# Kernel optimization log

Measured on AMD Instinct MI355X. Metric: run time of the kernel, lower is better.

## Reference

```python
import jax, jax.numpy as jnp
import numpy as np

EMBED = 1024
HEADS = 16
HIDDEN = 4 * EMBED
EPS = 1e-5


def layer_norm(x, g, b):
    mu = jnp.mean(x, axis=-1, keepdims=True)
    var = jnp.var(x, axis=-1, keepdims=True)
    return (x - mu) * jax.lax.rsqrt(var + EPS) * g + b


def setup_inputs() -> dict:
    key = jax.random.key(0)
    ks = jax.random.split(key, 8)
    s = EMBED ** -0.5
    return {
        "x": jax.random.normal(ks[0], (4, 2048, EMBED), dtype=jnp.float32),
        "ln1_g": jnp.ones((EMBED,), jnp.float32),
        "ln1_b": jnp.zeros((EMBED,), jnp.float32),
        "qkv_w": jax.random.normal(ks[1], (3 * EMBED, EMBED), jnp.float32) * s,
        "out_w": jax.random.normal(ks[2], (EMBED, EMBED), jnp.float32) * s,
        "out_b": jnp.zeros((EMBED,), jnp.float32),
        "ln2_g": jnp.ones((EMBED,), jnp.float32),
        "ln2_b": jnp.zeros((EMBED,), jnp.float32),
        "fc1_w": jax.random.normal(ks[3], (HIDDEN, EMBED), jnp.float32) * s,
        "fc1_b": jnp.zeros((HIDDEN,), jnp.float32),
        "fc2_w": jax.random.normal(ks[4], (EMBED, HIDDEN), jnp.float32) * (HIDDEN ** -0.5),
        "fc2_b": jnp.zeros((EMBED,), jnp.float32),
    }


def reference(x, ln1_g, ln1_b, qkv_w, out_w, out_b, ln2_g, ln2_b, fc1_w, fc1_b, fc2_w, fc2_b):
    B, N, C = x.shape
    hd = C // HEADS
    # --- attention (pre-LN); note: NO 1/sqrt(d) scaling, matching the source ---
    h = layer_norm(x, ln1_g, ln1_b)
    qkv = h @ qkv_w.T                                  # [B,N,3C]
    qkv = qkv.reshape(B, N, 3, HEADS, hd).transpose(2, 0, 3, 1, 4)
    q, k, v = qkv[0], qkv[1], qkv[2]                   # [B,H,N,hd]
    attn = jax.nn.softmax(jnp.einsum("bhqd,bhkd->bhqk", q, k), axis=-1)
    o = jnp.einsum("bhqk,bhkd->bhqd", attn, v)
    o = o.transpose(0, 2, 1, 3).reshape(B, N, C)
    x = x + o @ out_w.T + out_b
    # --- MLP (exact erf GELU, matching nn.GELU default) ---
    h = layer_norm(x, ln2_g, ln2_b)
    h = jax.nn.gelu(h @ fc1_w.T + fc1_b, approximate=False)
    x = x + h @ fc2_w.T + fc2_b
    return x
```

## Files before the change

kernel.cpp:

```cpp
#include <hip/hip_runtime.h>
#include <cstdint>


using short8 = __attribute__((ext_vector_type(8))) short;
using f32x4  = __attribute__((ext_vector_type(4))) float;
using f32x16 = __attribute__((ext_vector_type(16))) float;

#define EMBED  1024
#define HIDDEN 4096
#define SEQ    2048
#define NTOK   8192

__device__ __forceinline__ ushort f2bf(float x) {
  union { float f; uint32_t u; } v; v.f = x;
  uint32_t r = v.u + 0x7fffu + ((v.u >> 16) & 1u);
  return (ushort)(r >> 16);
}

__device__ __forceinline__ uint32_t pkbf(float lo, float hi) {
  uint32_t r;
  asm("v_cvt_pk_bf16_f32 %0, %1, %2" : "=v"(r) : "v"(lo), "v"(hi));
  return r;
}

__device__ __forceinline__ void gload16(const void* g, void* l) {
  __builtin_amdgcn_global_load_lds((__attribute__((address_space(1))) void*)(g),
                                   (__attribute__((address_space(3))) void*)(l), 16, 0, 0);
}

template<int N> __device__ __forceinline__ void vwait() {
  asm volatile("s_waitcnt vmcnt(%0)" :: "n"(N) : "memory");
}
__device__ __forceinline__ void fence_bar() {
  asm volatile("" ::: "memory");
  __builtin_amdgcn_s_barrier();
  asm volatile("" ::: "memory");
}

__device__ __forceinline__ f32x4 mfma16(short8 a, short8 b, f32x4 c) {
  return __builtin_amdgcn_mfma_f32_16x16x32_bf16(a, b, c, 0, 0, 0);
}
__device__ __forceinline__ f32x16 mfma32(short8 a, short8 b, f32x16 c) {
  return __builtin_amdgcn_mfma_f32_32x32x16_bf16(a, b, c, 0, 0, 0);
}
__device__ __forceinline__ f32x16 zero16() {
  f32x16 z = {0.f,0.f,0.f,0.f,0.f,0.f,0.f,0.f,0.f,0.f,0.f,0.f,0.f,0.f,0.f,0.f};
  return z;
}

__global__ __launch_bounds__(256) void cvt_bf16_kernel(const float* __restrict__ in,
                                                       ushort* __restrict__ out, int n4) {
  int i = blockIdx.x * 256 + threadIdx.x;
  if (i < n4) {
    float4 v = reinterpret_cast<const float4*>(in)[i];
    ushort4 o; o.x = f2bf(v.x); o.y = f2bf(v.y); o.z = f2bf(v.z); o.w = f2bf(v.w);
    reinterpret_cast<ushort4*>(out)[i] = o;
  }
}

__global__ __launch_bounds__(256) void ln_kernel(const float* __restrict__ x,
                                                 const float* __restrict__ g,
                                                 const float* __restrict__ b,
                                                 ushort* __restrict__ out) {
  const int row = blockIdx.x, tid = threadIdx.x;
  const float4 xv = reinterpret_cast<const float4*>(x + (size_t)row * EMBED)[tid];
  float s  = xv.x + xv.y + xv.z + xv.w;
  float s2 = xv.x*xv.x + xv.y*xv.y + xv.z*xv.z + xv.w*xv.w;
  #pragma unroll
  for (int off = 32; off >= 1; off >>= 1) { s += __shfl_xor(s, off); s2 += __shfl_xor(s2, off); }
  __shared__ float ps[4], ps2[4];
  if ((tid & 63) == 0) { ps[tid >> 6] = s; ps2[tid >> 6] = s2; }
  __syncthreads();
  s  = ps[0] + ps[1] + ps[2] + ps[3];
  s2 = ps2[0] + ps2[1] + ps2[2] + ps2[3];
  const float mu  = s * (1.f / EMBED);
  const float var = s2 * (1.f / EMBED) - mu * mu;
  const float rs  = rsqrtf(var + 1e-5f);
  const float4 gv = reinterpret_cast<const float4*>(g)[tid];
  const float4 bv = reinterpret_cast<const float4*>(b)[tid];
  ushort4 o;
  o.x = f2bf((xv.x - mu) * rs * gv.x + bv.x);
  o.y = f2bf((xv.y - mu) * rs * gv.y + bv.y);
  o.z = f2bf((xv.z - mu) * rs * gv.z + bv.z);
  o.w = f2bf((xv.w - mu) * rs * gv.w + bv.w);
  reinterpret_cast<ushort4*>(out + (size_t)row * EMBED)[tid] = o;
}

template<int EPI, bool SQ>
__global__ __launch_bounds__(512) void gemm256(const ushort* __restrict__ A,
                                               const ushort* __restrict__ B,
                                               const float* __restrict__ bias,
                                               const float* __restrict__ res,
                                               ushort* __restrict__ outb,
                                               float* __restrict__ outf,
                                               int M, int N, int K, int gx) {
  constexpr int BN   = SQ ? 256 : 128;
  constexpr int MP   = SQ ? 8 : 4;
  constexpr int NPH  = SQ ? 2 : 1;
  constexpr int LPT  = SQ ? 4 : 3;
  constexpr int NB   = LPT - 2;
  constexpr int ABUF = 256 * 32;
  constexpr int BBUF = BN * 32;
  __shared__ ushort lds[4][ABUF + BBUF];

  const int nwg = gridDim.x;
  const int b0  = blockIdx.x;
  const int bid = (b0 & 7) * (nwg >> 3) + (b0 >> 3);
  const int m0  = (bid % gx) * 256;
  const int n0  = (bid / gx) * BN;

  const int tid = threadIdx.x, lane = tid & 63, wave = tid >> 6;
  const int wm = (SQ ? (wave >> 2) : (wave >> 1)) * (MP * 16);
  const int wn = (SQ ? (wave & 3) : (wave & 1)) * 64;
  const int l15 = lane & 15, l4 = lane >> 4;
  const int NT = K >> 5;

  const ushort* aSrc[2];
  const ushort* bSrc[NB];
  #pragma unroll
  for (int rd = 0; rd < 2; ++rd) {
    const int slot = rd * 512 + tid;
    const int r = slot >> 2;
    const int cs = (slot & 3) ^ ((r >> 1) & 3);
    aSrc[rd] = A + (size_t)(m0 + r) * K + cs * 8;
  }
  #pragma unroll
  for (int rd = 0; rd < NB; ++rd) {
    const int slot = rd * 512 + tid;
    const int r = slot >> 2;
    const int cs = (slot & 3) ^ ((r >> 1) & 3);
    bSrc[rd] = B + (size_t)(n0 + r) * K + cs * 8;
  }
  auto stageA = [&](int buf, int rd) { gload16(aSrc[rd], &lds[buf][(rd * 512 + tid) * 8]); };
  auto stageB = [&](int buf, int rd) { gload16(bSrc[rd], &lds[buf][ABUF + (rd * 512 + tid) * 8]); };
  auto advance = [&]() {
    #pragma unroll
    for (int rd = 0; rd < 2; ++rd) aSrc[rd] += 32;
    #pragma unroll
    for (int rd = 0; rd < NB; ++rd) bSrc[rd] += 32;
  };

  #pragma unroll
  for (int t = 0; t < 3; ++t) {
    stageA(t, 0); stageA(t, 1);
    #pragma unroll
    for (int rd = 0; rd < NB; ++rd) stageB(t, rd);
    advance();
  }
  vwait<2 * LPT>();
  fence_bar();

  f32x4 acc[MP][4] = {};

  auto doTile = [&](int q, bool st, int wsel) {
    const ushort* bA = &lds[q][0];
    const ushort* bB = &lds[q][ABUF];
    const int sbuf = (q + 3) & 3;
    short8 bf[4];
    #pragma unroll
    for (int j = 0; j < 4; ++j) {
      const int rb = wn + j * 16 + l15;
      bf[j] = *reinterpret_cast<const short8*>(&bB[rb * 32 + ((l4 ^ ((rb >> 1) & 3)) * 8)]);
    }
    #pragma unroll
    for (int ph = 0; ph < NPH; ++ph) {
      short8 af[4];
      #pragma unroll
      for (int i = 0; i < 4; ++i) {
        const int ra = wm + (ph * 4 + i) * 16 + l15;
        af[i] = *reinterpret_cast<const short8*>(&bA[ra * 32 + ((l4 ^ ((ra >> 1) & 3)) * 8)]);
      }
      if (st) {
        if constexpr (SQ) {
          if (ph == 0) { stageA(sbuf, 0); stageA(sbuf, 1); }
          else         { stageB(sbuf, 0); stageB(sbuf, 1); }
        } else {
          stageA(sbuf, 0); stageA(sbuf, 1); stageB(sbuf, 0);
        }
      }
      fence_bar();
      __builtin_amdgcn_s_setprio(1);
      #pragma unroll
      for (int i = 0; i < 4; ++i)
        #pragma unroll
        for (int j = 0; j < 4; ++j)
          acc[ph * 4 + i][j] = mfma16(af[i], bf[j], acc[ph * 4 + i][j]);
      __builtin_amdgcn_s_setprio(0);
      if (ph == NPH - 1) {
        if (st) advance();
        if (wsel == 0)      vwait<2 * LPT>();
        else if (wsel == 1) vwait<LPT>();
        else if (wsel == 2) vwait<0>();
      }
      fence_bar();
    }
  };

  for (int u0 = 0; u0 < NT - 4; u0 += 4) {
    doTile(0, true, 0); doTile(1, true, 0); doTile(2, true, 0); doTile(3, true, 0);
  }
  doTile(0, true, 0); doTile(1, false, 1); doTile(2, false, 2); doTile(3, false, 3);

  #pragma unroll
  for (int i = 0; i < MP; ++i)
    #pragma unroll
    for (int j = 0; j < 4; ++j)
      #pragma unroll
      for (int r = 0; r < 4; ++r) {
        const int row = m0 + wm + i * 16 + l4 * 4 + r;
        const int col = n0 + wn + j * 16 + l15;
        const size_t idx = (size_t)row * N + col;
        float v = acc[i][j][r];
        if constexpr (EPI == 0) {
          outb[idx] = f2bf(v);
        } else if constexpr (EPI == 1) {
          outf[idx] = v + bias[col] + res[idx];
        } else {
          v += bias[col];
          v = 0.5f * v * (1.f + erff(v * 0.70710678118654752f));
          outb[idx] = f2bf(v);
        }
      }
}

#define KVB 64
#define NTT (SEQ / KVB)

__global__ __launch_bounds__(256, 2) void attn_kernel(const ushort* __restrict__ qk,
                                                      const ushort* __restrict__ vt,
                                                      ushort* __restrict__ outp) {
  const int tid = threadIdx.x, lane = tid & 63, wq = tid >> 6;
  const int hi = lane >> 5, lo = lane & 31;
  const int b = blockIdx.x >> 4, h = blockIdx.x & 15;
  const int q0 = blockIdx.y * 256;

  __shared__ ushort sK[2][64 * 64];
  __shared__ ushort sVt[2][64 * 64];
  __shared__ float sBc[4][2][32];

  short8 qf[2][4];
  #pragma unroll
  for (int s = 0; s < 2; ++s)
    #pragma unroll
    for (int kc = 0; kc < 4; ++kc)
      qf[s][kc] = *reinterpret_cast<const short8*>(
          qk + (size_t)(b * SEQ + q0 + wq * 64 + s * 32 + lo) * 2048 + h * 64 + kc * 16 + hi * 8);

  auto STAGE = [&](int bb, int kt) {
    #pragma unroll
    for (int i = 0; i < 2; ++i) {
      const int slot = i * 256 + tid;
      const int r = slot >> 3;
      const int c = (slot & 7) ^ (r & 7);
      gload16(qk + (size_t)(b * SEQ + kt + r) * 2048 + 1024 + h * 64 + c * 8,
              &sK[bb][(i * 256 + wq * 64) * 8]);
      gload16(vt + (size_t)(h * 64 + r) * 8192 + b * SEQ + kt + c * 8,
              &sVt[bb][(i * 256 + wq * 64) * 8]);
    }
  };

  f32x16 acc[2][2];
  #pragma unroll
  for (int s = 0; s < 2; ++s) { acc[s][0] = zero16(); acc[s][1] = zero16(); }
  float mst[2] = {-1e30f, -1e30f}, lst[2] = {0.f, 0.f};

  STAGE(0, 0);
  for (int t = 0; t < NTT; ++t) {
    const int cur = t & 1;
    __syncthreads();
    if (t + 1 < NTT) STAGE(cur ^ 1, (t + 1) * KVB);

    short8 kf[2][4];
    #pragma unroll
    for (int kvb = 0; kvb < 2; ++kvb)
      #pragma unroll
      for (int kc = 0; kc < 4; ++kc) {
        const int row = kvb * 32 + lo, ch = kc * 2 + hi;
        kf[kvb][kc] = *reinterpret_cast<const short8*>(
            &sK[cur][(row * 8 + (ch ^ (row & 7))) * 8]);
      }

    short8 pa[2][4];
    #pragma unroll
    for (int s = 0; s < 2; ++s) {
      f32x16 st[2];
      #pragma unroll
      for (int kvb = 0; kvb < 2; ++kvb) {
        f32x16 tq = zero16();
        tq = mfma32(kf[kvb][0], qf[s][0], tq);
        tq = mfma32(kf[kvb][1], qf[s][1], tq);
        tq = mfma32(kf[kvb][2], qf[s][2], tq);
        tq = mfma32(kf[kvb][3], qf[s][3], tq);
        st[kvb] = tq;
      }
      float pm = fmaxf(st[0][0], st[0][1]);
      #pragma unroll
      for (int r = 2; r < 16; ++r) pm = fmaxf(pm, st[0][r]);
      #pragma unroll
      for (int r = 0; r < 16; ++r) pm = fmaxf(pm, st[1][r]);
      pm = fmaxf(pm, __shfl_xor(pm, 32));
      if (__any(pm > mst[s] + 8.f)) {
        const float mn = fmaxf(mst[s], pm);
        const float al = __expf(mst[s] - mn);
        mst[s] = mn; lst[s] *= al;
        sBc[wq][s][lo] = al;
        asm volatile("s_waitcnt lgkmcnt(0)" ::: "memory");
        #pragma unroll
        for (int g = 0; g < 4; ++g) {
          const f32x4 a4 = *reinterpret_cast<const f32x4*>(&sBc[wq][s][g * 8 + hi * 4]);
          #pragma unroll
          for (int j = 0; j < 4; ++j) {
            acc[s][0][g * 4 + j] *= a4[j];
            acc[s][1][g * 4 + j] *= a4[j];
          }
        }
      }
      #pragma unroll
      for (int kvb = 0; kvb < 2; ++kvb)
        #pragma unroll
        for (int r = 0; r < 16; ++r)
          st[kvb][r] = __expf(st[kvb][r] - mst[s]);
      {
        const f32x16 sv = st[0] + st[1];
        float sum = ((sv[0] + sv[1]) + (sv[2] + sv[3])) + ((sv[4] + sv[5]) + (sv[6] + sv[7]))
                  + ((sv[8] + sv[9]) + (sv[10] + sv[11])) + ((sv[12] + sv[13]) + (sv[14] + sv[15]));
        sum += __shfl_xor(sum, 32);
        lst[s] += sum;
      }
      #pragma unroll
      for (int kvb = 0; kvb < 2; ++kvb)
        #pragma unroll
        for (int f = 0; f < 2; ++f) {
          uint32_t wa = pkbf(st[kvb][f * 8 + 0], st[kvb][f * 8 + 1]);
          uint32_t wb = pkbf(st[kvb][f * 8 + 2], st[kvb][f * 8 + 3]);
          uint32_t wc = pkbf(st[kvb][f * 8 + 4], st[kvb][f * 8 + 5]);
          uint32_t wd = pkbf(st[kvb][f * 8 + 6], st[kvb][f * 8 + 7]);
          asm volatile("v_permlane32_swap_b32 %0, %1" : "+v"(wa), "+v"(wc));
          asm volatile("v_permlane32_swap_b32 %0, %1" : "+v"(wb), "+v"(wd));
          union { uint32_t w[4]; short8 v; } u;
          u.w[0] = wa; u.w[1] = wb; u.w[2] = wc; u.w[3] = wd;
          pa[s][kvb * 2 + f] = u.v;
        }
    }

    #pragma unroll
    for (int db = 0; db < 2; ++db) {
      short8 vb[4];
      #pragma unroll
      for (int k4 = 0; k4 < 4; ++k4) {
        const int row = db * 32 + lo, ch = k4 * 2 + hi;
        vb[k4] = *reinterpret_cast<const short8*>(
            &sVt[cur][(row * 8 + (ch ^ (row & 7))) * 8]);
      }
      #pragma unroll
      for (int s = 0; s < 2; ++s) {
        acc[s][db] = mfma32(pa[s][0], vb[0], acc[s][db]);
        acc[s][db] = mfma32(pa[s][1], vb[1], acc[s][db]);
        acc[s][db] = mfma32(pa[s][2], vb[2], acc[s][db]);
        acc[s][db] = mfma32(pa[s][3], vb[3], acc[s][db]);
      }
    }
  }

  #pragma unroll
  for (int s = 0; s < 2; ++s) sBc[wq][s][lo] = 1.f / lst[s];
  asm volatile("s_waitcnt lgkmcnt(0)" ::: "memory");
  #pragma unroll
  for (int s = 0; s < 2; ++s)
    #pragma unroll
    for (int g = 0; g < 4; ++g) {
      const f32x4 r4 = *reinterpret_cast<const f32x4*>(&sBc[wq][s][g * 8 + hi * 4]);
      #pragma unroll
      for (int j = 0; j < 4; ++j) {
        const int qrow = q0 + wq * 64 + s * 32 + g * 8 + hi * 4 + j;
        #pragma unroll
        for (int db = 0; db < 2; ++db)
          outp[(size_t)(b * SEQ + qrow) * EMBED + h * 64 + db * 32 + lo] =
              f2bf(acc[s][db][g * 4 + j] * r4[j]);
      }
    }
}

extern "C" void kernel_launch(void* const* d_in, const int* in_sizes, int n_in,
                              void* d_out, int out_size, void* d_ws, size_t ws_size,
                              hipStream_t stream) {
  const float* x     = (const float*)d_in[0];
  const float* ln1_g = (const float*)d_in[1];
  const float* ln1_b = (const float*)d_in[2];
  const float* qkv_w = (const float*)d_in[3];
  const float* out_w = (const float*)d_in[4];
  const float* out_b = (const float*)d_in[5];
  const float* ln2_g = (const float*)d_in[6];
  const float* ln2_b = (const float*)d_in[7];
  const float* fc1_w = (const float*)d_in[8];
  const float* fc1_b = (const float*)d_in[9];
  const float* fc2_w = (const float*)d_in[10];
  const float* fc2_b = (const float*)d_in[11];
  float* out = (float*)d_out;
  char* ws = (char*)d_ws;

  ushort* qkvw = (ushort*)(ws);
  ushort* outw = (ushort*)(ws + 6291456);
  ushort* fc1w = (ushort*)(ws + 8388608);
  ushort* fc2w = (ushort*)(ws + 16777216);
  float*  x1   = (float*) (ws + 25165824);
  ushort* hbuf = (ushort*)(ws + 58720256);
  ushort* qkbuf= (ushort*)(ws + 75497472);
  ushort* vtbuf= (ushort*)(ws + 109051904);
  ushort* obuf = (ushort*)(ws + 125829120);
  ushort* gbuf = qkbuf;

  cvt_bf16_kernel<<<3072, 256, 0, stream>>>(qkv_w, qkvw, 3 * EMBED * EMBED / 4);
  cvt_bf16_kernel<<<1024, 256, 0, stream>>>(out_w, outw, EMBED * EMBED / 4);
  cvt_bf16_kernel<<<4096, 256, 0, stream>>>(fc1_w, fc1w, HIDDEN * EMBED / 4);
  cvt_bf16_kernel<<<4096, 256, 0, stream>>>(fc2_w, fc2w, EMBED * HIDDEN / 4);

  ln_kernel<<<NTOK, 256, 0, stream>>>(x, ln1_g, ln1_b, hbuf);
  gemm256<0, true><<<256, 512, 0, stream>>>(hbuf, qkvw, nullptr, nullptr,
                                            qkbuf, nullptr, NTOK, 2 * EMBED, EMBED, 32);
  gemm256<0, false><<<256, 512, 0, stream>>>(qkvw + 2048 * 1024, hbuf, nullptr, nullptr,
                                             vtbuf, nullptr, EMBED, NTOK, EMBED, 4);
  attn_kernel<<<dim3(64, 8), 256, 0, stream>>>(qkbuf, vtbuf, obuf);
  gemm256<1, false><<<256, 512, 0, stream>>>(obuf, outw, out_b, x,
                                             nullptr, x1, NTOK, EMBED, EMBED, 32);
  ln_kernel<<<NTOK, 256, 0, stream>>>(x1, ln2_g, ln2_b, hbuf);
  gemm256<2, true><<<512, 512, 0, stream>>>(hbuf, fc1w, fc1_b, nullptr,
                                            gbuf, nullptr, NTOK, HIDDEN, EMBED, 32);
  gemm256<1, false><<<256, 512, 0, stream>>>(gbuf, fc2w, fc2_b, x1,
                                             nullptr, out, NTOK, EMBED, HIDDEN, 32);
}
```

Before: 415.5 us.

## Restructure GEMM pipeline to double-buffered 64-wide K steps

The GEMM mainloop moves from a 4-deep ring of 32-wide K tiles to two buffers, each holding a 64-wide K step split into two 32-wide halves. Loads for the next step are spread across the four MFMA phases, with waits after each half, so there are fewer pipeline stages but more work per stage. LDS fragment offsets are now computed once up front instead of in every tile. The trade-off is a shallower prefetch depth, which may expose more global-load latency, against fewer barriers per unit of K and less per-tile address arithmetic.

```diff
diff --git a/kernel.cpp b/kernel.cpp
--- a/kernel.cpp
+++ b/kernel.cpp
@@ -87,21 +87,20 @@
 }
 
 template<int EPI, bool SQ>
-__global__ __launch_bounds__(512) void gemm256(const ushort* __restrict__ A,
-                                               const ushort* __restrict__ B,
-                                               const float* __restrict__ bias,
-                                               const float* __restrict__ res,
-                                               ushort* __restrict__ outb,
-                                               float* __restrict__ outf,
-                                               int M, int N, int K, int gx) {
-  constexpr int BN   = SQ ? 256 : 128;
-  constexpr int MP   = SQ ? 8 : 4;
-  constexpr int NPH  = SQ ? 2 : 1;
-  constexpr int LPT  = SQ ? 4 : 3;
-  constexpr int NB   = LPT - 2;
-  constexpr int ABUF = 256 * 32;
-  constexpr int BBUF = BN * 32;
-  __shared__ ushort lds[4][ABUF + BBUF];
+__global__ __launch_bounds__(512) void gemm64(const ushort* __restrict__ A,
+                                              const ushort* __restrict__ B,
+                                              const float* __restrict__ bias,
+                                              const float* __restrict__ res,
+                                              ushort* __restrict__ outb,
+                                              float* __restrict__ outf,
+                                              int M, int N, int K, int gx) {
+  constexpr int BN  = SQ ? 256 : 128;
+  constexpr int MP  = SQ ? 8 : 4;
+  constexpr int NBR = SQ ? 2 : 1;
+  constexpr int AH  = 256 * 32;
+  constexpr int BH  = BN * 32;
+  constexpr int KH  = AH + BH;
+  __shared__ ushort lds[2][2 * KH];
 
   const int nwg = gridDim.x;
   const int b0  = blockIdx.x;
@@ -113,93 +112,152 @@
   const int wm = (SQ ? (wave >> 2) : (wave >> 1)) * (MP * 16);
   const int wn = (SQ ? (wave & 3) : (wave & 1)) * 64;
   const int l15 = lane & 15, l4 = lane >> 4;
-  const int NT = K >> 5;
-
-  const ushort* aSrc[2];
-  const ushort* bSrc[NB];
+  const int NT = K >> 6;
+
+  const ushort* aS[2];
+  const ushort* bS[NBR];
   #pragma unroll
   for (int rd = 0; rd < 2; ++rd) {
     const int slot = rd * 512 + tid;
     const int r = slot >> 2;
     const int cs = (slot & 3) ^ ((r >> 1) & 3);
-    aSrc[rd] = A + (size_t)(m0 + r) * K + cs * 8;
-  }
-  #pragma unroll
-  for (int rd = 0; rd < NB; ++rd) {
+    aS[rd] = A + (size_t)(m0 + r) * K + cs * 8;
+  }
+  #pragma unroll
+  for (int rd = 0; rd < NBR; ++rd) {
     const int slot = rd * 512 + tid;
     const int r = slot >> 2;
     const int cs = (slot & 3) ^ ((r >> 1) & 3);
-    bSrc[rd] = B + (size_t)(n0 + r) * K + cs * 8;
-  }
-  auto stageA = [&](int buf, int rd) { gload16(aSrc[rd], &lds[buf][(rd * 512 + tid) * 8]); };
-  auto stageB = [&](int buf, int rd) { gload16(bSrc[rd], &lds[buf][ABUF + (rd * 512 + tid) * 8]); };
+    bS[rd] = B + (size_t)(n0 + r) * K + cs * 8;
+  }
+  auto stA = [&](ushort* buf, int half, int rd) {
+    gload16(aS[rd] + half * 32, buf + half * KH + (rd * 512 + tid) * 8);
+  };
+  auto stB = [&](ushort* buf, int half, int rd) {
+    gload16(bS[rd] + half * 32, buf + AH + half * KH + (rd * 512 + tid) * 8);
+  };
   auto advance = [&]() {
     #pragma unroll
-    for (int rd = 0; rd < 2; ++rd) aSrc[rd] += 32;
-    #pragma unroll
-    for (int rd = 0; rd < NB; ++rd) bSrc[rd] += 32;
+    for (int rd = 0; rd < 2; ++rd) aS[rd] += 64;
+    #pragma unroll
+    for (int rd = 0; rd < NBR; ++rd) bS[rd] += 64;
   };
 
-  #pragma unroll
-  for (int t = 0; t < 3; ++t) {
-    stageA(t, 0); stageA(t, 1);
-    #pragma unroll
-    for (int rd = 0; rd < NB; ++rd) stageB(t, rd);
-    advance();
-  }
-  vwait<2 * LPT>();
+  int aOff[MP], bOff[4];
+  #pragma unroll
+  for (int i = 0; i < MP; ++i) {
+    const int ra = wm + i * 16 + l15;
+    aOff[i] = ra * 32 + ((l4 ^ ((ra >> 1) & 3)) * 8);
+  }
+  #pragma unroll
+  for (int j = 0; j < 4; ++j) {
+    const int rb = wn + j * 16 + l15;
+    bOff[j] = rb * 32 + ((l4 ^ ((rb >> 1) & 3)) * 8);
+  }
+
+  ushort* p0 = &lds[0][0];
+  ushort* p1 = &lds[1][0];
+  stA(p0, 0, 0); stA(p0, 0, 1);
+  #pragma unroll
+  for (int rd = 0; rd < NBR; ++rd) stB(p0, 0, rd);
+  stA(p0, 1, 0); stA(p0, 1, 1);
+  #pragma unroll
+  for (int rd = 0; rd < NBR; ++rd) stB(p0, 1, rd);
+  advance();
+  vwait<SQ ? 4 : 3>();
   fence_bar();
 
   f32x4 acc[MP][4] = {};
 
-  auto doTile = [&](int q, bool st, int wsel) {
-    const ushort* bA = &lds[q][0];
-    const ushort* bB = &lds[q][ABUF];
-    const int sbuf = (q + 3) & 3;
-    short8 bf[4];
-    #pragma unroll
-    for (int j = 0; j < 4; ++j) {
-      const int rb = wn + j * 16 + l15;
-      bf[j] = *reinterpret_cast<const short8*>(&bB[rb * 32 + ((l4 ^ ((rb >> 1) & 3)) * 8)]);
+  auto TILE = [&](ushort* cur, ushort* nxt, bool st, bool tail) {
+    short8 af[4], bf[4];
+    if constexpr (SQ) {
+      #pragma unroll
+      for (int j = 0; j < 4; ++j) bf[j] = *reinterpret_cast<const short8*>(cur + AH + bOff[j]);
+      #pragma unroll
+      for (int i = 0; i < 4; ++i) af[i] = *reinterpret_cast<const short8*>(cur + aOff[i]);
+      if (st) { stA(nxt, 0, 0); stA(nxt, 0, 1); }
+      fence_bar();
+      __builtin_amdgcn_s_setprio(1);
+      #pragma unroll
+      for (int i = 0; i < 4; ++i)
+        #pragma unroll
+        for (int j = 0; j < 4; ++j) acc[i][j] = mfma16(af[i], bf[j], acc[i][j]);
+      __builtin_amdgcn_s_setprio(0);
+      fence_bar();
+      #pragma unroll
+      for (int i = 0; i < 4; ++i) af[i] = *reinterpret_cast<const short8*>(cur + aOff[4 + i]);
+      if (st) { stB(nxt, 0, 0); stB(nxt, 0, 1); }
+      fence_bar();
+      __builtin_amdgcn_s_setprio(1);
+      #pragma unroll
+      for (int i = 0; i < 4; ++i)
+        #pragma unroll
+        for (int j = 0; j < 4; ++j) acc[4 + i][j] = mfma16(af[i], bf[j], acc[4 + i][j]);
+      __builtin_amdgcn_s_setprio(0);
+      if (!tail) vwait<4>(); else vwait<0>();
+      fence_bar();
+      #pragma unroll
+      for (int j = 0; j < 4; ++j) bf[j] = *reinterpret_cast<const short8*>(cur + KH + AH + bOff[j]);
+      #pragma unroll
+      for (int i = 0; i < 4; ++i) af[i] = *reinterpret_cast<const short8*>(cur + KH + aOff[i]);
+      if (st) { stA(nxt, 1, 0); stA(nxt, 1, 1); }
+      fence_bar();
+      __builtin_amdgcn_s_setprio(1);
+      #pragma unroll
+      for (int i = 0; i < 4; ++i)
+        #pragma unroll
+        for (int j = 0; j < 4; ++j) acc[i][j] = mfma16(af[i], bf[j], acc[i][j]);
+      __builtin_amdgcn_s_setprio(0);
+      fence_bar();
+      #pragma unroll
+      for (int i = 0; i < 4; ++i) af[i] = *reinterpret_cast<const short8*>(cur + KH + aOff[4 + i]);
+      if (st) { stB(nxt, 1, 0); stB(nxt, 1, 1); }
+      fence_bar();
+      __builtin_amdgcn_s_setprio(1);
+      #pragma unroll
+      for (int i = 0; i < 4; ++i)
+        #pragma unroll
+        for (int j = 0; j < 4; ++j) acc[4 + i][j] = mfma16(af[i], bf[j], acc[4 + i][j]);
+      __builtin_amdgcn_s_setprio(0);
+      if (!tail) vwait<4>();
+      fence_bar();
+    } else {
+      #pragma unroll
+      for (int j = 0; j < 4; ++j) bf[j] = *reinterpret_cast<const short8*>(cur + AH + bOff[j]);
+      #pragma unroll
+      for (int i = 0; i < 4; ++i) af[i] = *reinterpret_cast<const short8*>(cur + aOff[i]);
+      if (st) { stA(nxt, 0, 0); stA(nxt, 0, 1); stB(nxt, 0, 0); }
+      fence_bar();
+      __builtin_amdgcn_s_setprio(1);
+      #pragma unroll
+      for (int i = 0; i < 4; ++i)
+        #pragma unroll
+        for (int j = 0; j < 4; ++j) acc[i][j] = mfma16(af[i], bf[j], acc[i][j]);
+      __builtin_amdgcn_s_setprio(0);
+      if (!tail) vwait<3>(); else vwait<0>();
+      fence_bar();
+      #pragma unroll
+      for (int j = 0; j < 4; ++j) bf[j] = *reinterpret_cast<const short8*>(cur + KH + AH + bOff[j]);
+      #pragma unroll
+      for (int i = 0; i < 4; ++i) af[i] = *reinterpret_cast<const short8*>(cur + KH + aOff[i]);
+      if (st) { stA(nxt, 1, 0); stA(nxt, 1, 1); stB(nxt, 1, 0); }
+      fence_bar();
+      __builtin_amdgcn_s_setprio(1);
+      #pragma unroll
+      for (int i = 0; i < 4; ++i)
+        #pragma unroll
+        for (int j = 0; j < 4; ++j) acc[i][j] = mfma16(af[i], bf[j], acc[i][j]);
+      __builtin_amdgcn_s_setprio(0);
+      if (!tail) vwait<3>();
+      fence_bar();
     }
-    #pragma unroll
-    for (int ph = 0; ph < NPH; ++ph) {
-      short8 af[4];
-      #pragma unroll
-      for (int i = 0; i < 4; ++i) {
-        const int ra = wm + (ph * 4 + i) * 16 + l15;
-        af[i] = *reinterpret_cast<const short8*>(&bA[ra * 32 + ((l4 ^ ((ra >> 1) & 3)) * 8)]);
-      }
-      if (st) {
-        if constexpr (SQ) {
-          if (ph == 0) { stageA(sbuf, 0); stageA(sbuf, 1); }
-          else         { stageB(sbuf, 0); stageB(sbuf, 1); }
-        } else {
-          stageA(sbuf, 0); stageA(sbuf, 1); stageB(sbuf, 0);
-        }
-      }
-      fence_bar();
-      __builtin_amdgcn_s_setprio(1);
-      #pragma unroll
-      for (int i = 0; i < 4; ++i)
-        #pragma unroll
-        for (int j = 0; j < 4; ++j)
-          acc[ph * 4 + i][j] = mfma16(af[i], bf[j], acc[ph * 4 + i][j]);
-      __builtin_amdgcn_s_setprio(0);
-      if (ph == NPH - 1) {
-        if (st) advance();
-        if (wsel == 0)      vwait<2 * LPT>();
-        else if (wsel == 1) vwait<LPT>();
-        else if (wsel == 2) vwait<0>();
-      }
-      fence_bar();
-    }
+    if (st) advance();
   };
 
-  for (int u0 = 0; u0 < NT - 4; u0 += 4) {
-    doTile(0, true, 0); doTile(1, true, 0); doTile(2, true, 0); doTile(3, true, 0);
-  }
-  doTile(0, true, 0); doTile(1, false, 1); doTile(2, false, 2); doTile(3, false, 3);
+  for (int t = 0; t < NT - 2; t += 2) { TILE(p0, p1, true, false); TILE(p1, p0, true, false); }
+  TILE(p0, p1, true, false);
+  TILE(p1, p0, false, true);
 
   #pragma unroll
   for (int i = 0; i < MP; ++i)
@@ -416,16 +474,16 @@
   cvt_bf16_kernel<<<4096, 256, 0, stream>>>(fc2_w, fc2w, EMBED * HIDDEN / 4);
 
   ln_kernel<<<NTOK, 256, 0, stream>>>(x, ln1_g, ln1_b, hbuf);
-  gemm256<0, true><<<256, 512, 0, stream>>>(hbuf, qkvw, nullptr, nullptr,
-                                            qkbuf, nullptr, NTOK, 2 * EMBED, EMBED, 32);
-  gemm256<0, false><<<256, 512, 0, stream>>>(qkvw + 2048 * 1024, hbuf, nullptr, nullptr,
-                                             vtbuf, nullptr, EMBED, NTOK, EMBED, 4);
+  gemm64<0, true><<<256, 512, 0, stream>>>(hbuf, qkvw, nullptr, nullptr,
+                                           qkbuf, nullptr, NTOK, 2 * EMBED, EMBED, 32);
+  gemm64<0, false><<<256, 512, 0, stream>>>(qkvw + 2048 * 1024, hbuf, nullptr, nullptr,
+                                            vtbuf, nullptr, EMBED, NTOK, EMBED, 4);
   attn_kernel<<<dim3(64, 8), 256, 0, stream>>>(qkbuf, vtbuf, obuf);
-  gemm256<1, false><<<256, 512, 0, stream>>>(obuf, outw, out_b, x,
-                                             nullptr, x1, NTOK, EMBED, EMBED, 32);
+  gemm64<1, false><<<256, 512, 0, stream>>>(obuf, outw, out_b, x,
+                                            nullptr, x1, NTOK, EMBED, EMBED, 32);
   ln_kernel<<<NTOK, 256, 0, stream>>>(x1, ln2_g, ln2_b, hbuf);
-  gemm256<2, true><<<512, 512, 0, stream>>>(hbuf, fc1w, fc1_b, nullptr,
-                                            gbuf, nullptr, NTOK, HIDDEN, EMBED, 32);
-  gemm256<1, false><<<256, 512, 0, stream>>>(gbuf, fc2w, fc2_b, x1,
-                                             nullptr, out, NTOK, EMBED, HIDDEN, 32);
-}
+  gemm64<2, true><<<512, 512, 0, stream>>>(hbuf, fc1w, fc1_b, nullptr,
+                                           gbuf, nullptr, NTOK, HIDDEN, EMBED, 32);
+  gemm64<1, false><<<256, 512, 0, stream>>>(gbuf, fc2w, fc2_b, x1,
+                                            nullptr, out, NTOK, EMBED, HIDDEN, 32);
+}
```

Result: no change. 411.3 us (-1.0%).

## Switch GEMMs to 32x32x16 MFMA with double-buffered 64-wide K tiles

Applied to the files above, without the earlier changes.

Rewrites the shared GEMM kernel to use 32x32x16 bf16 MFMA instructions instead of 16x16x32, which cuts LDS fragment reads per FLOP and the instruction count. The pipeline changes from a 4-deep ring of 32-wide K tiles to two buffers, each holding a 64-wide K tile split into two halves, with loads for the next tile issued per half. Output indexing is updated for the 32x32 accumulator layout. Prefetch depth is lower, so more load latency may be exposed, and accumulator register pressure changes.

```diff
diff --git a/kernel.cpp b/kernel.cpp
--- a/kernel.cpp
+++ b/kernel.cpp
@@ -37,9 +37,6 @@
   asm volatile("" ::: "memory");
 }
 
-__device__ __forceinline__ f32x4 mfma16(short8 a, short8 b, f32x4 c) {
-  return __builtin_amdgcn_mfma_f32_16x16x32_bf16(a, b, c, 0, 0, 0);
-}
 __device__ __forceinline__ f32x16 mfma32(short8 a, short8 b, f32x16 c) {
   return __builtin_amdgcn_mfma_f32_32x32x16_bf16(a, b, c, 0, 0, 0);
 }
@@ -87,21 +84,22 @@
 }
 
 template<int EPI, bool SQ>
-__global__ __launch_bounds__(512) void gemm256(const ushort* __restrict__ A,
-                                               const ushort* __restrict__ B,
-                                               const float* __restrict__ bias,
-                                               const float* __restrict__ res,
-                                               ushort* __restrict__ outb,
-                                               float* __restrict__ outf,
-                                               int M, int N, int K, int gx) {
+__global__ __launch_bounds__(512) void gemm32(const ushort* __restrict__ A,
+                                              const ushort* __restrict__ B,
+                                              const float* __restrict__ bias,
+                                              const float* __restrict__ res,
+                                              ushort* __restrict__ outb,
+                                              float* __restrict__ outf,
+                                              int M, int N, int K, int gx) {
   constexpr int BN   = SQ ? 256 : 128;
-  constexpr int MP   = SQ ? 8 : 4;
-  constexpr int NPH  = SQ ? 2 : 1;
-  constexpr int LPT  = SQ ? 4 : 3;
-  constexpr int NB   = LPT - 2;
-  constexpr int ABUF = 256 * 32;
-  constexpr int BBUF = BN * 32;
-  __shared__ ushort lds[4][ABUF + BBUF];
+  constexpr int MPOS = SQ ? 4 : 2;
+  constexpr int NPOS = 2;
+  constexpr int BBR  = SQ ? 2 : 1;
+  constexpr int LPH  = 2 + BBR;
+  constexpr int AH   = 256 * 32;
+  constexpr int BH   = BN * 32;
+  constexpr int KH   = AH + BH;
+  __shared__ ushort lds[2][2 * KH];
 
   const int nwg = gridDim.x;
   const int b0  = blockIdx.x;
@@ -110,107 +108,125 @@
   const int n0  = (bid / gx) * BN;
 
   const int tid = threadIdx.x, lane = tid & 63, wave = tid >> 6;
-  const int wm = (SQ ? (wave >> 2) : (wave >> 1)) * (MP * 16);
+  const int wm = (SQ ? (wave >> 2) : (wave >> 1)) * (MPOS * 32);
   const int wn = (SQ ? (wave & 3) : (wave & 1)) * 64;
-  const int l15 = lane & 15, l4 = lane >> 4;
-  const int NT = K >> 5;
-
-  const ushort* aSrc[2];
-  const ushort* bSrc[NB];
+  const int l31 = lane & 31, l32 = lane >> 5;
+  const int NT = K >> 6;
+
+  const ushort* aS[2];
+  const ushort* bS[BBR];
   #pragma unroll
   for (int rd = 0; rd < 2; ++rd) {
     const int slot = rd * 512 + tid;
     const int r = slot >> 2;
     const int cs = (slot & 3) ^ ((r >> 1) & 3);
-    aSrc[rd] = A + (size_t)(m0 + r) * K + cs * 8;
-  }
-  #pragma unroll
-  for (int rd = 0; rd < NB; ++rd) {
+    aS[rd] = A + (size_t)(m0 + r) * K + cs * 8;
+  }
+  #pragma unroll
+  for (int rd = 0; rd < BBR; ++rd) {
     const int slot = rd * 512 + tid;
     const int r = slot >> 2;
     const int cs = (slot & 3) ^ ((r >> 1) & 3);
-    bSrc[rd] = B + (size_t)(n0 + r) * K + cs * 8;
-  }
-  auto stageA = [&](int buf, int rd) { gload16(aSrc[rd], &lds[buf][(rd * 512 + tid) * 8]); };
-  auto stageB = [&](int buf, int rd) { gload16(bSrc[rd], &lds[buf][ABUF + (rd * 512 + tid) * 8]); };
+    bS[rd] = B + (size_t)(n0 + r) * K + cs * 8;
+  }
+  auto stA = [&](ushort* buf, int half, int rd) {
+    gload16(aS[rd] + half * 32, buf + half * KH + (rd * 512 + tid) * 8);
+  };
+  auto stB = [&](ushort* buf, int half, int rd) {
+    gload16(bS[rd] + half * 32, buf + AH + half * KH + (rd * 512 + tid) * 8);
+  };
+  auto stageHalf = [&](ushort* buf, int half) {
+    stA(buf, half, 0); stA(buf, half, 1);
+    #pragma unroll
+    for (int rd = 0; rd < BBR; ++rd) stB(buf, half, rd);
+  };
   auto advance = [&]() {
     #pragma unroll
-    for (int rd = 0; rd < 2; ++rd) aSrc[rd] += 32;
-    #pragma unroll
-    for (int rd = 0; rd < NB; ++rd) bSrc[rd] += 32;
-  };
-
-  #pragma unroll
-  for (int t = 0; t < 3; ++t) {
-    stageA(t, 0); stageA(t, 1);
-    #pragma unroll
-    for (int rd = 0; rd < NB; ++rd) stageB(t, rd);
-    advance();
-  }
-  vwait<2 * LPT>();
+    for (int rd = 0; rd < 2; ++rd) aS[rd] += 64;
+    #pragma unroll
+    for (int rd = 0; rd < BBR; ++rd) bS[rd] += 64;
+  };
+
+  int aOff[MPOS][2], bOff[NPOS][2];
+  #pragma unroll
+  for (int mp = 0; mp < MPOS; ++mp) {
+    const int ra = wm + mp * 32 + l31;
+    #pragma unroll
+    for (int s = 0; s < 2; ++s)
+      aOff[mp][s] = ra * 32 + (((2 * s + l32) ^ ((ra >> 1) & 3)) * 8);
+  }
+  #pragma unroll
+  for (int np = 0; np < NPOS; ++np) {
+    const int rb = wn + np * 32 + l31;
+    #pragma unroll
+    for (int s = 0; s < 2; ++s)
+      bOff[np][s] = rb * 32 + (((2 * s + l32) ^ ((rb >> 1) & 3)) * 8);
+  }
+
+  ushort* p0 = &lds[0][0];
+  ushort* p1 = &lds[1][0];
+  stageHalf(p0, 0);
+  stageHalf(p0, 1);
+  advance();
+  vwait<LPH>();
   fence_bar();
 
-  f32x4 acc[MP][4] = {};
-
-  auto doTile = [&](int q, bool st, int wsel) {
-    const ushort* bA = &lds[q][0];
-    const ushort* bB = &lds[q][ABUF];
-    const int sbuf = (q + 3) & 3;
-    short8 bf[4];
-    #pragma unroll
-    for (int j = 0; j < 4; ++j) {
-      const int rb = wn + j * 16 + l15;
-      bf[j] = *reinterpret_cast<const short8*>(&bB[rb * 32 + ((l4 ^ ((rb >> 1) & 3)) * 8)]);
-    }
-    #pragma unroll
-    for (int ph = 0; ph < NPH; ++ph) {
-      short8 af[4];
-      #pragma unroll
-      for (int i = 0; i < 4; ++i) {
-        const int ra = wm + (ph * 4 + i) * 16 + l15;
-        af[i] = *reinterpret_cast<const short8*>(&bA[ra * 32 + ((l4 ^ ((ra >> 1) & 3)) * 8)]);
-      }
-      if (st) {
-        if constexpr (SQ) {
-          if (ph == 0) { stageA(sbuf, 0); stageA(sbuf, 1); }
-          else         { stageB(sbuf, 0); stageB(sbuf, 1); }
-        } else {
-          stageA(sbuf, 0); stageA(sbuf, 1); stageB(sbuf, 0);
-        }
-      }
-      fence_bar();
-      __builtin_amdgcn_s_setprio(1);
-      #pragma unroll
-      for (int i = 0; i < 4; ++i)
+  f32x16 acc[MPOS][NPOS];
+  #pragma unroll
+  for (int mp = 0; mp < MPOS; ++mp)
+    #pragma unroll
+    for (int np = 0; np < NPOS; ++np) acc[mp][np] = zero16();
+
+  auto PHASE = [&](ushort* cur, ushort* nxt, int half, bool st, int wsel) {
+    const ushort* hA = cur + half * KH;
+    const ushort* hB = hA + AH;
+    short8 af[MPOS][2], bf[NPOS][2];
+    #pragma unroll
+    for (int mp = 0; mp < MPOS; ++mp)
+      #pragma unroll
+      for (int s = 0; s < 2; ++s)
+        af[mp][s] = *reinterpret_cast<const short8*>(hA + aOff[mp][s]);
+    #pragma unroll
+    for (int np = 0; np < NPOS; ++np)
+      #pragma unroll
+      for (int s = 0; s < 2; ++s)
+        bf[np][s] = *reinterpret_cast<const short8*>(hB + bOff[np][s]);
+    if (st) stageHalf(nxt, half);
+    fence_bar();
+    __builtin_amdgcn_s_setprio(1);
+    #pragma unroll
+    for (int s = 0; s < 2; ++s)
+      #pragma unroll
+      for (int mp = 0; mp < MPOS; ++mp)
         #pragma unroll
-        for (int j = 0; j < 4; ++j)
-          acc[ph * 4 + i][j] = mfma16(af[i], bf[j], acc[ph * 4 + i][j]);
-      __builtin_amdgcn_s_setprio(0);
-      if (ph == NPH - 1) {
-        if (st) advance();
-        if (wsel == 0)      vwait<2 * LPT>();
-        else if (wsel == 1) vwait<LPT>();
-        else if (wsel == 2) vwait<0>();
-      }
-      fence_bar();
-    }
-  };
-
-  for (int u0 = 0; u0 < NT - 4; u0 += 4) {
-    doTile(0, true, 0); doTile(1, true, 0); doTile(2, true, 0); doTile(3, true, 0);
-  }
-  doTile(0, true, 0); doTile(1, false, 1); doTile(2, false, 2); doTile(3, false, 3);
-
-  #pragma unroll
-  for (int i = 0; i < MP; ++i)
-    #pragma unroll
-    for (int j = 0; j < 4; ++j)
-      #pragma unroll
-      for (int r = 0; r < 4; ++r) {
-        const int row = m0 + wm + i * 16 + l4 * 4 + r;
-        const int col = n0 + wn + j * 16 + l15;
+        for (int np = 0; np < NPOS; ++np)
+          acc[mp][np] = mfma32(af[mp][s], bf[np][s], acc[mp][np]);
+    __builtin_amdgcn_s_setprio(0);
+    if (wsel == 0)      vwait<LPH>();
+    else if (wsel == 1) vwait<0>();
+    fence_bar();
+  };
+
+  auto TILE = [&](ushort* cur, ushort* nxt, bool st, bool tail) {
+    PHASE(cur, nxt, 0, st, tail ? 1 : 0);
+    PHASE(cur, nxt, 1, st, tail ? 2 : 0);
+    if (st) advance();
+  };
+
+  for (int t = 0; t < NT - 2; t += 2) { TILE(p0, p1, true, false); TILE(p1, p0, true, false); }
+  TILE(p0, p1, true, false);
+  TILE(p1, p0, false, true);
+
+  #pragma unroll
+  for (int mp = 0; mp < MPOS; ++mp)
+    #pragma unroll
+    for (int np = 0; np < NPOS; ++np)
+      #pragma unroll
+      for (int reg = 0; reg < 16; ++reg) {
+        const int row = m0 + wm + mp * 32 + (reg & 3) + 8 * (reg >> 2) + 4 * l32;
+        const int col = n0 + wn + np * 32 + l31;
         const size_t idx = (size_t)row * N + col;
-        float v = acc[i][j][r];
+        float v = acc[mp][np][reg];
         if constexpr (EPI == 0) {
           outb[idx] = f2bf(v);
         } else if constexpr (EPI == 1) {
@@ -416,16 +432,16 @@
   cvt_bf16_kernel<<<4096, 256, 0, stream>>>(fc2_w, fc2w, EMBED * HIDDEN / 4);
 
   ln_kernel<<<NTOK, 256, 0, stream>>>(x, ln1_g, ln1_b, hbuf);
-  gemm256<0, true><<<256, 512, 0, stream>>>(hbuf, qkvw, nullptr, nullptr,
-                                            qkbuf, nullptr, NTOK, 2 * EMBED, EMBED, 32);
-  gemm256<0, false><<<256, 512, 0, stream>>>(qkvw + 2048 * 1024, hbuf, nullptr, nullptr,
-                                             vtbuf, nullptr, EMBED, NTOK, EMBED, 4);
+  gemm32<0, true><<<256, 512, 0, stream>>>(hbuf, qkvw, nullptr, nullptr,
+                                           qkbuf, nullptr, NTOK, 2 * EMBED, EMBED, 32);
+  gemm32<0, false><<<256, 512, 0, stream>>>(qkvw + 2048 * 1024, hbuf, nullptr, nullptr,
+                                            vtbuf, nullptr, EMBED, NTOK, EMBED, 4);
   attn_kernel<<<dim3(64, 8), 256, 0, stream>>>(qkbuf, vtbuf, obuf);
-  gemm256<1, false><<<256, 512, 0, stream>>>(obuf, outw, out_b, x,
-                                             nullptr, x1, NTOK, EMBED, EMBED, 32);
+  gemm32<1, false><<<256, 512, 0, stream>>>(obuf, outw, out_b, x,
+                                            nullptr, x1, NTOK, EMBED, EMBED, 32);
   ln_kernel<<<NTOK, 256, 0, stream>>>(x1, ln2_g, ln2_b, hbuf);
-  gemm256<2, true><<<512, 512, 0, stream>>>(hbuf, fc1w, fc1_b, nullptr,
-                                            gbuf, nullptr, NTOK, HIDDEN, EMBED, 32);
-  gemm256<1, false><<<256, 512, 0, stream>>>(gbuf, fc2w, fc2_b, x1,
-                                             nullptr, out, NTOK, EMBED, HIDDEN, 32);
-}
+  gemm32<2, true><<<512, 512, 0, stream>>>(hbuf, fc1w, fc1_b, nullptr,
+                                           gbuf, nullptr, NTOK, HIDDEN, EMBED, 32);
+  gemm32<1, false><<<256, 512, 0, stream>>>(gbuf, fc2w, fc2_b, x1,
+                                            nullptr, out, NTOK, EMBED, HIDDEN, 32);
+}
```

Result: slower. 427.3 us (+2.8%).

## Restructure GEMM into K=64 double-buffered 8-phase ping-pong schedule

Applied to the files above, without the earlier changes.

Replaces the 4-stage K=32 GEMM pipeline with a 2-buffer K=64 tile design, where each tile is split into 128-row halves and processed in four MFMA sub-phases. LDS reads, global-to-LDS staging and MFMA batches are interleaved with explicit barriers and lgkmcnt waits. The aim is to halve the barriers per K element and hide LDS and global latency behind MFMA work. It uses an 8-wide XOR swizzle for the wider rows. The added barriers and the shallower prefetch depth risk exposing global-load latency.

```diff
diff --git a/kernel.cpp b/kernel.cpp
--- a/kernel.cpp
+++ b/kernel.cpp
@@ -30,6 +30,9 @@
 
 template<int N> __device__ __forceinline__ void vwait() {
   asm volatile("s_waitcnt vmcnt(%0)" :: "n"(N) : "memory");
+}
+__device__ __forceinline__ void lgkm0() {
+  asm volatile("s_waitcnt lgkmcnt(0)" ::: "memory");
 }
 __device__ __forceinline__ void fence_bar() {
   asm volatile("" ::: "memory");
@@ -87,21 +90,21 @@
 }
 
 template<int EPI, bool SQ>
-__global__ __launch_bounds__(512) void gemm256(const ushort* __restrict__ A,
-                                               const ushort* __restrict__ B,
-                                               const float* __restrict__ bias,
-                                               const float* __restrict__ res,
-                                               ushort* __restrict__ outb,
-                                               float* __restrict__ outf,
-                                               int M, int N, int K, int gx) {
+__global__ __launch_bounds__(512) void gemm8p(const ushort* __restrict__ A,
+                                              const ushort* __restrict__ B,
+                                              const float* __restrict__ bias,
+                                              const float* __restrict__ res,
+                                              ushort* __restrict__ outb,
+                                              float* __restrict__ outf,
+                                              int M, int N, int K, int gx) {
   constexpr int BN   = SQ ? 256 : 128;
-  constexpr int MP   = SQ ? 8 : 4;
-  constexpr int NPH  = SQ ? 2 : 1;
-  constexpr int LPT  = SQ ? 4 : 3;
-  constexpr int NB   = LPT - 2;
-  constexpr int ABUF = 256 * 32;
-  constexpr int BBUF = BN * 32;
-  __shared__ ushort lds[4][ABUF + BBUF];
+  constexpr int NH   = SQ ? 4 : 3;
+  constexpr int HSZ  = 128 * 64;
+  constexpr int MPOS = SQ ? 8 : 4;
+  constexpr int MI   = SQ ? 4 : 2;
+  constexpr int NBH  = SQ ? 2 : 1;
+  constexpr int LPT  = SQ ? 8 : 6;
+  __shared__ ushort lds[2][NH * HSZ];
 
   const int nwg = gridDim.x;
   const int b0  = blockIdx.x;
@@ -110,107 +113,153 @@
   const int n0  = (bid / gx) * BN;
 
   const int tid = threadIdx.x, lane = tid & 63, wave = tid >> 6;
-  const int wm = (SQ ? (wave >> 2) : (wave >> 1)) * (MP * 16);
-  const int wn = (SQ ? (wave & 3) : (wave & 1)) * 64;
   const int l15 = lane & 15, l4 = lane >> 4;
-  const int NT = K >> 5;
-
-  const ushort* aSrc[2];
-  const ushort* bSrc[NB];
-  #pragma unroll
-  for (int rd = 0; rd < 2; ++rd) {
-    const int slot = rd * 512 + tid;
-    const int r = slot >> 2;
-    const int cs = (slot & 3) ^ ((r >> 1) & 3);
-    aSrc[rd] = A + (size_t)(m0 + r) * K + cs * 8;
-  }
-  #pragma unroll
-  for (int rd = 0; rd < NB; ++rd) {
-    const int slot = rd * 512 + tid;
-    const int r = slot >> 2;
-    const int cs = (slot & 3) ^ ((r >> 1) & 3);
-    bSrc[rd] = B + (size_t)(n0 + r) * K + cs * 8;
-  }
-  auto stageA = [&](int buf, int rd) { gload16(aSrc[rd], &lds[buf][(rd * 512 + tid) * 8]); };
-  auto stageB = [&](int buf, int rd) { gload16(bSrc[rd], &lds[buf][ABUF + (rd * 512 + tid) * 8]); };
+  const int wm = SQ ? (wave >> 2) * 128 : (wave >> 1) * 64;
+  const int wn = SQ ? (wave & 3) * 64 : (wave & 1) * 64;
+  const int NT = K >> 6;
+
+  const int aRegIdx = wave >> 2;
+  const int lraB = SQ ? 0 : ((wave >> 1) & 1) * 64;
+  const int bRegIdx = SQ ? (2 + ((wave & 3) >> 1)) : 2;
+  const int lcB  = (wave & 1) * 64;
+
+  int aOff[2][MI][2], bOff[2][2][2];
+  #pragma unroll
+  for (int ms = 0; ms < 2; ++ms)
+    #pragma unroll
+    for (int i = 0; i < MI; ++i)
+      #pragma unroll
+      for (int ks = 0; ks < 2; ++ks) {
+        const int lr = lraB + ms * (SQ ? 64 : 32) + i * 16 + l15;
+        aOff[ms][i][ks] = lr * 64 + (((ks * 4 + l4) ^ (lr & 7)) * 8);
+      }
+  #pragma unroll
+  for (int ns = 0; ns < 2; ++ns)
+    #pragma unroll
+    for (int j = 0; j < 2; ++j)
+      #pragma unroll
+      for (int ks = 0; ks < 2; ++ks) {
+        const int c = lcB + ns * 32 + j * 16 + l15;
+        bOff[ns][j][ks] = c * 64 + (((ks * 4 + l4) ^ (c & 7)) * 8);
+      }
+
+  const ushort* aP[2][2];
+  const ushort* bP[NBH][2];
+  #pragma unroll
+  for (int h = 0; h < 2; ++h)
+    #pragma unroll
+    for (int rd = 0; rd < 2; ++rd) {
+      const int slot = rd * 512 + tid, r = slot >> 3;
+      aP[h][rd] = A + (size_t)(m0 + h * 128 + r) * K + (((slot & 7) ^ (r & 7)) * 8);
+    }
+  #pragma unroll
+  for (int h = 0; h < NBH; ++h)
+    #pragma unroll
+    for (int rd = 0; rd < 2; ++rd) {
+      const int slot = rd * 512 + tid, r = slot >> 3;
+      bP[h][rd] = B + (size_t)(n0 + h * 128 + r) * K + (((slot & 7) ^ (r & 7)) * 8);
+    }
+  auto stA = [&](int par, int h, int rd) {
+    gload16(aP[h][rd], &lds[par][h * HSZ + (rd * 512 + tid) * 8]);
+  };
+  auto stB = [&](int par, int h, int rd) {
+    gload16(bP[h][rd], &lds[par][(2 + h) * HSZ + (rd * 512 + tid) * 8]);
+  };
   auto advance = [&]() {
     #pragma unroll
-    for (int rd = 0; rd < 2; ++rd) aSrc[rd] += 32;
-    #pragma unroll
-    for (int rd = 0; rd < NB; ++rd) bSrc[rd] += 32;
-  };
-
-  #pragma unroll
-  for (int t = 0; t < 3; ++t) {
-    stageA(t, 0); stageA(t, 1);
-    #pragma unroll
-    for (int rd = 0; rd < NB; ++rd) stageB(t, rd);
+    for (int h = 0; h < 2; ++h) { aP[h][0] += 64; aP[h][1] += 64; }
+    #pragma unroll
+    for (int h = 0; h < NBH; ++h) { bP[h][0] += 64; bP[h][1] += 64; }
+  };
+
+  #pragma unroll
+  for (int t = 0; t < 2; ++t) {
+    #pragma unroll
+    for (int h = 0; h < NBH; ++h) { stB(t, h, 0); stB(t, h, 1); }
+    #pragma unroll
+    for (int h = 0; h < 2; ++h) { stA(t, h, 0); stA(t, h, 1); }
     advance();
   }
-  vwait<2 * LPT>();
+  vwait<LPT>();
   fence_bar();
 
-  f32x4 acc[MP][4] = {};
-
-  auto doTile = [&](int q, bool st, int wsel) {
-    const ushort* bA = &lds[q][0];
-    const ushort* bB = &lds[q][ABUF];
-    const int sbuf = (q + 3) & 3;
-    short8 bf[4];
-    #pragma unroll
-    for (int j = 0; j < 4; ++j) {
-      const int rb = wn + j * 16 + l15;
-      bf[j] = *reinterpret_cast<const short8*>(&bB[rb * 32 + ((l4 ^ ((rb >> 1) & 3)) * 8)]);
-    }
-    #pragma unroll
-    for (int ph = 0; ph < NPH; ++ph) {
-      short8 af[4];
-      #pragma unroll
-      for (int i = 0; i < 4; ++i) {
-        const int ra = wm + (ph * 4 + i) * 16 + l15;
-        af[i] = *reinterpret_cast<const short8*>(&bA[ra * 32 + ((l4 ^ ((ra >> 1) & 3)) * 8)]);
-      }
-      if (st) {
-        if constexpr (SQ) {
-          if (ph == 0) { stageA(sbuf, 0); stageA(sbuf, 1); }
-          else         { stageB(sbuf, 0); stageB(sbuf, 1); }
-        } else {
-          stageA(sbuf, 0); stageA(sbuf, 1); stageB(sbuf, 0);
-        }
-      }
-      fence_bar();
-      __builtin_amdgcn_s_setprio(1);
-      #pragma unroll
-      for (int i = 0; i < 4; ++i)
+  f32x4 acc[MPOS][4] = {};
+  short8 af[MI][2], bf[2][2][2];
+
+  auto RDA = [&](const ushort* LA, int ms) {
+    #pragma unroll
+    for (int i = 0; i < MI; ++i)
+      #pragma unroll
+      for (int ks = 0; ks < 2; ++ks)
+        af[i][ks] = *reinterpret_cast<const short8*>(LA + aOff[ms][i][ks]);
+  };
+  auto RDB = [&](const ushort* LB, int ns) {
+    #pragma unroll
+    for (int j = 0; j < 2; ++j)
+      #pragma unroll
+      for (int ks = 0; ks < 2; ++ks)
+        bf[ns][j][ks] = *reinterpret_cast<const short8*>(LB + bOff[ns][j][ks]);
+  };
+  auto MM = [&](int ms, int ns) {
+    __builtin_amdgcn_s_setprio(1);
+    #pragma unroll
+    for (int ks = 0; ks < 2; ++ks)
+      #pragma unroll
+      for (int i = 0; i < MI; ++i)
         #pragma unroll
-        for (int j = 0; j < 4; ++j)
-          acc[ph * 4 + i][j] = mfma16(af[i], bf[j], acc[ph * 4 + i][j]);
-      __builtin_amdgcn_s_setprio(0);
-      if (ph == NPH - 1) {
-        if (st) advance();
-        if (wsel == 0)      vwait<2 * LPT>();
-        else if (wsel == 1) vwait<LPT>();
-        else if (wsel == 2) vwait<0>();
-      }
-      fence_bar();
-    }
-  };
-
-  for (int u0 = 0; u0 < NT - 4; u0 += 4) {
-    doTile(0, true, 0); doTile(1, true, 0); doTile(2, true, 0); doTile(3, true, 0);
+        for (int j = 0; j < 2; ++j)
+          acc[ms * MI + i][ns * 2 + j] =
+              mfma16(af[i][ks], bf[ns][j][ks], acc[ms * MI + i][ns * 2 + j]);
+    __builtin_amdgcn_s_setprio(0);
+  };
+
+  auto TILE = [&](int par, bool st, int wmode) {
+    const ushort* LA = &lds[par][aRegIdx * HSZ];
+    const ushort* LB = &lds[par][bRegIdx * HSZ];
+    RDA(LA, 0); RDB(LB, 0);
+    fence_bar(); lgkm0();
+    MM(0, 0);
+    fence_bar();
+    RDB(LB, 1);
+    fence_bar(); lgkm0();
+    MM(0, 1);
+    fence_bar();
+    RDA(LA, 1);
+    if (st) {
+      #pragma unroll
+      for (int h = 0; h < NBH; ++h) { stB(par, h, 0); stB(par, h, 1); }
+    }
+    fence_bar(); lgkm0();
+    MM(1, 1);
+    fence_bar();
+    if (st) {
+      #pragma unroll
+      for (int h = 0; h < 2; ++h) { stA(par, h, 0); stA(par, h, 1); }
+    }
+    MM(1, 0);
+    if (wmode == 0)      vwait<LPT>();
+    else if (wmode == 1) vwait<0>();
+    fence_bar();
+    if (st) advance();
+  };
+
+  for (int u = 0; u < NT - 2; u += 2) {
+    TILE(0, true, 0);
+    TILE(1, (u + 1 < NT - 2), (u + 1 == NT - 2) ? 1 : 0);
   }
-  doTile(0, true, 0); doTile(1, false, 1); doTile(2, false, 2); doTile(3, false, 3);
-
-  #pragma unroll
-  for (int i = 0; i < MP; ++i)
-    #pragma unroll
-    for (int j = 0; j < 4; ++j)
+  TILE(0, false, 1);
+  TILE(1, false, 2);
+
+  #pragma unroll
+  for (int mi = 0; mi < MPOS; ++mi)
+    #pragma unroll
+    for (int nj = 0; nj < 4; ++nj)
       #pragma unroll
       for (int r = 0; r < 4; ++r) {
-        const int row = m0 + wm + i * 16 + l4 * 4 + r;
-        const int col = n0 + wn + j * 16 + l15;
+        const int row = m0 + wm + mi * 16 + l4 * 4 + r;
+        const int col = n0 + wn + nj * 16 + l15;
         const size_t idx = (size_t)row * N + col;
-        float v = acc[i][j][r];
+        float v = acc[mi][nj][r];
         if constexpr (EPI == 0) {
           outb[idx] = f2bf(v);
         } else if constexpr (EPI == 1) {
@@ -416,16 +465,16 @@
   cvt_bf16_kernel<<<4096, 256, 0, stream>>>(fc2_w, fc2w, EMBED * HIDDEN / 4);
 
   ln_kernel<<<NTOK, 256, 0, stream>>>(x, ln1_g, ln1_b, hbuf);
-  gemm256<0, true><<<256, 512, 0, stream>>>(hbuf, qkvw, nullptr, nullptr,
-                                            qkbuf, nullptr, NTOK, 2 * EMBED, EMBED, 32);
-  gemm256<0, false><<<256, 512, 0, stream>>>(qkvw + 2048 * 1024, hbuf, nullptr, nullptr,
-                                             vtbuf, nullptr, EMBED, NTOK, EMBED, 4);
+  gemm8p<0, true><<<256, 512, 0, stream>>>(hbuf, qkvw, nullptr, nullptr,
+                                           qkbuf, nullptr, NTOK, 2 * EMBED, EMBED, 32);
+  gemm8p<0, false><<<256, 512, 0, stream>>>(qkvw + 2048 * 1024, hbuf, nullptr, nullptr,
+                                            vtbuf, nullptr, EMBED, NTOK, EMBED, 4);
   attn_kernel<<<dim3(64, 8), 256, 0, stream>>>(qkbuf, vtbuf, obuf);
-  gemm256<1, false><<<256, 512, 0, stream>>>(obuf, outw, out_b, x,
-                                             nullptr, x1, NTOK, EMBED, EMBED, 32);
+  gemm8p<1, false><<<256, 512, 0, stream>>>(obuf, outw, out_b, x,
+                                            nullptr, x1, NTOK, EMBED, EMBED, 32);
   ln_kernel<<<NTOK, 256, 0, stream>>>(x1, ln2_g, ln2_b, hbuf);
-  gemm256<2, true><<<512, 512, 0, stream>>>(hbuf, fc1w, fc1_b, nullptr,
-                                            gbuf, nullptr, NTOK, HIDDEN, EMBED, 32);
-  gemm256<1, false><<<256, 512, 0, stream>>>(gbuf, fc2w, fc2_b, x1,
-                                             nullptr, out, NTOK, EMBED, HIDDEN, 32);
-}
+  gemm8p<2, true><<<512, 512, 0, stream>>>(hbuf, fc1w, fc1_b, nullptr,
+                                           gbuf, nullptr, NTOK, HIDDEN, EMBED, 32);
+  gemm8p<1, false><<<256, 512, 0, stream>>>(gbuf, fc2w, fc2_b, x1,
+                                            nullptr, out, NTOK, EMBED, HIDDEN, 32);
+}
```

New measurement: 413.9 us. No clear change (-0.4%).
